# Kernel tuning notes

Hardware: AMD Instinct MI355X
Metric: run time of the kernel (lower is better)

## Reference

```python
import jax, jax.numpy as jnp
import numpy as np
import math

D_MODEL = 1024
N_HEAD = 16

def setup_inputs() -> dict:
    key = jax.random.key(0)
    ks = jax.random.split(key, 9)
    d = D_MODEL
    s = 0.02
    return {
        "x": jax.random.normal(ks[0], (4, 2048, d), dtype=jnp.float32),
        "Wq": jax.random.normal(ks[1], (d, d), dtype=jnp.float32) * s,
        "bq": jnp.zeros((d,), dtype=jnp.float32),
        "Wk": jax.random.normal(ks[2], (d, d), dtype=jnp.float32) * s,
        "bk": jnp.zeros((d,), dtype=jnp.float32),
        "Wv": jax.random.normal(ks[3], (d, d), dtype=jnp.float32) * s,
        "bv": jnp.zeros((d,), dtype=jnp.float32),
        "Wo": jax.random.normal(ks[4], (d, d), dtype=jnp.float32) * s,
        "bo": jnp.zeros((d,), dtype=jnp.float32),
    }

def reference(x, Wq, bq, Wk, bk, Wv, bv, Wo, bo):
    B, S, D = x.shape
    H = N_HEAD
    hd = D // H
    # linear projections (torch nn.Linear: x @ W.T + b), split heads -> [B,H,S,hd]
    def proj(W, b):
        return (jnp.einsum('bsd,ed->bse', x, W) + b).reshape(B, S, H, hd).transpose(0, 2, 1, 3)
    q = proj(Wq, bq)
    k = proj(Wk, bk)
    v = proj(Wv, bv)
    scale = 1.0 / math.sqrt(hd)
    att = jnp.einsum('bhqd,bhkd->bhqk', q, k) * scale  # [B,H,S,S]
    causal = jnp.tril(jnp.ones((S, S), dtype=bool))
    att = jnp.where(causal, att, jnp.float32(-jnp.inf))
    att = jax.nn.softmax(att, axis=-1)
    y = jnp.einsum('bhqk,bhkd->bhqd', att, v)  # [B,H,S,hd]
    y = y.transpose(0, 2, 1, 3).reshape(B, S, D)
    y = jnp.einsum('bsd,ed->bse', y, Wo) + bo  # dropout is identity in eval
    return y
```

## Files before the change

### kernel.cpp

```cpp
#include <hip/hip_runtime.h>

typedef unsigned short u16;
typedef __attribute__((ext_vector_type(4))) float f32x4;
typedef __attribute__((ext_vector_type(8))) __bf16 bf16x8;
typedef __attribute__((ext_vector_type(4))) unsigned int u32x4;

#define SEQ 2048
#define DMODEL 1024
#define HD 64
#define QKV_ELEMS 8388608

__device__ __forceinline__ u16 f2bf(float f) {
  unsigned int u = __builtin_bit_cast(unsigned int, f);
  u += 0x7FFFu + ((u >> 16) & 1u);
  return (u16)(u >> 16);
}

__device__ __forceinline__ void gl2lds16(const u16* g, u16* l) {
  __builtin_amdgcn_global_load_lds(
      (__attribute__((address_space(1))) void*)g,
      (__attribute__((address_space(3))) void*)l, 16, 0, 0);
}

__device__ __forceinline__ f32x4 mfma_bf(bf16x8 a, bf16x8 b, f32x4 c) {
  return __builtin_amdgcn_mfma_f32_16x16x32_bf16(a, b, c, 0, 0, 0);
}

__device__ __forceinline__ void lgkm0() {
  __asm__ volatile("s_waitcnt lgkmcnt(0)" ::: "memory");
}

__global__ __launch_bounds__(256) void prep(
    const float* __restrict__ x, const float* __restrict__ wq,
    const float* __restrict__ wk, const float* __restrict__ wv,
    const float* __restrict__ wo, u16* __restrict__ xb,
    u16* __restrict__ wqkvb, u16* __restrict__ wob) {
  int idx = blockIdx.x * 256 + threadIdx.x;
  const float* src;
  u16* dst;
  if (idx < 2097152) {
    src = x + (size_t)idx * 4;
    dst = xb + (size_t)idx * 4;
  } else {
    int j = idx - 2097152;
    int seg = j >> 18;
    int off = (j & 262143) * 4;
    if (seg == 0)      { src = wq + off; dst = wqkvb + off; }
    else if (seg == 1) { src = wk + off; dst = wqkvb + 1048576 + off; }
    else if (seg == 2) { src = wv + off; dst = wqkvb + 2097152 + off; }
    else               { src = wo + off; dst = wob + off; }
  }
  float4 f = *(const float4*)src;
  ushort4 o;
  o.x = f2bf(f.x); o.y = f2bf(f.y); o.z = f2bf(f.z); o.w = f2bf(f.w);
  *(ushort4*)dst = o;
}

template <int MODE>
__global__ __launch_bounds__(256) void gemm_bt(
    const u16* __restrict__ A, const u16* __restrict__ Bt,
    const float* __restrict__ b0, const float* __restrict__ b1,
    const float* __restrict__ b2, u16* __restrict__ outb,
    float* __restrict__ outf, int Ndim) {
  __shared__ u16 lS[8192];
  u16* lA = lS;
  u16* lB = lS + 4096;
  const int tid = threadIdx.x;
  const int w = tid >> 6, L = tid & 63;
  const int quad = L >> 4, lane16 = L & 15;
  const int wm = w >> 1, wn = w & 1;
  const int bm = blockIdx.x * 128, bn = blockIdx.y * 128;
  const int K = 1024;

  f32x4 acc[4][4];
  for (int i = 0; i < 4; ++i)
    for (int j = 0; j < 4; ++j)
      for (int r = 0; r < 4; ++r) acc[i][j][r] = 0.f;

  const int srow = L >> 2, scol = (L & 3) * 8;
  const u16* Ag = A + (size_t)(bm + w * 16 + srow) * K + scol;
  const u16* Bg = Bt + (size_t)(bn + w * 16 + srow) * K + scol;
  u16* lA0 = &lA[(w * 16) * 32];
  u16* lA1 = &lA[(64 + w * 16) * 32];
  u16* lB0 = &lB[(w * 16) * 32];
  u16* lB1 = &lB[(64 + w * 16) * 32];

  for (int k0 = 0; k0 < K; k0 += 32) {
    __syncthreads();
    gl2lds16(Ag + k0, lA0);
    gl2lds16(Ag + k0 + 64 * K, lA1);
    gl2lds16(Bg + k0, lB0);
    gl2lds16(Bg + k0 + 64 * K, lB1);
    __syncthreads();
    bf16x8 af[4], bfr[4];
    for (int mt = 0; mt < 4; ++mt)
      af[mt] = __builtin_bit_cast(
          bf16x8, *(const u32x4*)&lA[(wm * 64 + mt * 16 + lane16) * 32 + quad * 8]);
    for (int nt = 0; nt < 4; ++nt)
      bfr[nt] = __builtin_bit_cast(
          bf16x8, *(const u32x4*)&lB[(wn * 64 + nt * 16 + lane16) * 32 + quad * 8]);
    for (int mt = 0; mt < 4; ++mt)
      for (int nt = 0; nt < 4; ++nt)
        acc[mt][nt] = mfma_bf(af[mt], bfr[nt], acc[mt][nt]);
  }

  if (MODE == 0) {
    __syncthreads();
    const int n0 = bn + wn * 64;
    const int which = n0 >> 10;
    const int nn0 = n0 & 1023;
    const int h2 = nn0 >> 6;
    const int b = bm >> 11;
    const int bh = b * 16 + h2;
    const int sbase = (bm & 2047) + wm * 64;
    const float* bp = (which == 0) ? b0 : (which == 1) ? b1 : b2;
    const float scl = (which == 0) ? 0.125f : 1.0f;
    float bias[4];
    for (int nt = 0; nt < 4; ++nt) bias[nt] = bp[nn0 + nt * 16 + lane16];
    u16* buf = lS + w * 1152;

    for (int mt = 0; mt < 4; ++mt) {
      for (int nt = 0; nt < 4; ++nt)
        for (int r = 0; r < 4; ++r)
          buf[(quad * 4 + r) * 72 + nt * 16 + lane16] =
              f2bf((acc[mt][nt][r] + bias[nt]) * scl);
      lgkm0();
      const int sloc = sbase + mt * 16;
      if (which < 2) {
        const int sr = L >> 2, c = L & 3;
        u32x4 v0 = *(const u32x4*)&buf[sr * 72 + c * 16];
        u32x4 v1 = *(const u32x4*)&buf[sr * 72 + c * 16 + 8];
        u16* g = outb + (size_t)which * QKV_ELEMS +
                 ((size_t)bh * SEQ + sloc + sr) * HD + c * 16;
        *(u32x4*)g = v0;
        *(u32x4*)(g + 8) = v1;
      } else {
        u16 tmp[16] __attribute__((aligned(16)));
        for (int r = 0; r < 16; ++r) tmp[r] = buf[r * 72 + L];
        u16* g = outb + (size_t)2 * QKV_ELEMS +
                 ((size_t)bh * HD + L) * SEQ + sloc;
        *(u32x4*)g = *(const u32x4*)tmp;
        *(u32x4*)(g + 8) = *(const u32x4*)(tmp + 8);
      }
      lgkm0();
    }
  } else {
    for (int nt = 0; nt < 4; ++nt) {
      int n = bn + wn * 64 + nt * 16 + lane16;
      float bias = b0[n];
      for (int mt = 0; mt < 4; ++mt) {
        int m0 = bm + wm * 64 + mt * 16 + quad * 4;
        for (int r = 0; r < 4; ++r) {
          int m = m0 + r;
          outf[(size_t)m * Ndim + n] = acc[mt][nt][r] + bias;
        }
      }
    }
  }
}

__global__ __launch_bounds__(256, 2) void attn(
    const u16* __restrict__ Qb, const u16* __restrict__ Kb,
    const u16* __restrict__ VTb, u16* __restrict__ Yb) {
  __shared__ u16 lK[2][64 * 72];
  __shared__ u16 lVT[2][64 * 72];
  __shared__ u16 lP[4][32 * 72];
  const int tid = threadIdx.x;
  const int w = tid >> 6, L = tid & 63;
  const int quad = L >> 4, lane16 = L & 15;
  const int bh = blockIdx.y;
  const int b = bh >> 4, h = bh & 15;
  const int kr = tid >> 2, c = tid & 3;
  const u16* Kbase = Kb + (size_t)bh * SEQ * HD;
  const u16* VTbase = VTb + (size_t)bh * HD * SEQ;

  for (int phase = 0; phase < 2; ++phase) {
    const int qi = (phase == 0) ? (int)blockIdx.x : 15 - (int)blockIdx.x;
    const int qb = qi * 128;
    const int ntiles = 2 * qi + 2;
    const int wqmin = qb + w * 32;
    const int wqmax = wqmin + 31;

    u32x4 qf[2][2];
    for (int mt = 0; mt < 2; ++mt)
      for (int kh = 0; kh < 2; ++kh)
        qf[mt][kh] = *(const u32x4*)(Qb +
            ((size_t)bh * SEQ + qb + w * 32 + mt * 16 + lane16) * HD +
            kh * 32 + quad * 8);

    f32x4 o[2][4];
    float lsum[2][4];
    for (int mt = 0; mt < 2; ++mt)
      for (int r = 0; r < 4; ++r) lsum[mt][r] = 0.f;
    for (int mt = 0; mt < 2; ++mt)
      for (int dt = 0; dt < 4; ++dt)
        for (int r = 0; r < 4; ++r) o[mt][dt][r] = 0.f;

    u32x4 ka0, ka1, va0, va1;
    {
      const u16* ks = Kbase + (size_t)kr * HD + c * 16;
      ka0 = *(const u32x4*)ks;
      ka1 = *(const u32x4*)(ks + 8);
      const u16* vs = VTbase + (size_t)kr * SEQ + c * 16;
      va0 = *(const u32x4*)vs;
      va1 = *(const u32x4*)(vs + 8);
    }

    for (int it = 0; it < ntiles; ++it) {
      const int cur = it & 1;
      const int kj0 = it * 64;
      *(u32x4*)&lK[cur][kr * 72 + c * 16] = ka0;
      *(u32x4*)&lK[cur][kr * 72 + c * 16 + 8] = ka1;
      *(u32x4*)&lVT[cur][kr * 72 + c * 16] = va0;
      *(u32x4*)&lVT[cur][kr * 72 + c * 16 + 8] = va1;
      __syncthreads();
      if (it + 1 < ntiles) {
        const int kn = (it + 1) * 64;
        const u16* ks = Kbase + (size_t)(kn + kr) * HD + c * 16;
        ka0 = *(const u32x4*)ks;
        ka1 = *(const u32x4*)(ks + 8);
        const u16* vs = VTbase + (size_t)kr * SEQ + kn + c * 16;
        va0 = *(const u32x4*)vs;
        va1 = *(const u32x4*)(vs + 8);
      }
      if (kj0 > wqmax) continue;

      f32x4 s[2][4];
      for (int mt = 0; mt < 2; ++mt)
        for (int nt = 0; nt < 4; ++nt)
          for (int r = 0; r < 4; ++r) s[mt][nt][r] = 0.f;
      for (int nt = 0; nt < 4; ++nt) {
        bf16x8 k0 = __builtin_bit_cast(
            bf16x8, *(const u32x4*)&lK[cur][(nt * 16 + lane16) * 72 + quad * 8]);
        bf16x8 k1 = __builtin_bit_cast(
            bf16x8, *(const u32x4*)&lK[cur][(nt * 16 + lane16) * 72 + 32 + quad * 8]);
        for (int mt = 0; mt < 2; ++mt) {
          s[mt][nt] = mfma_bf(__builtin_bit_cast(bf16x8, qf[mt][0]), k0, s[mt][nt]);
          s[mt][nt] = mfma_bf(__builtin_bit_cast(bf16x8, qf[mt][1]), k1, s[mt][nt]);
        }
      }
      if (kj0 + 63 > wqmin) {
        for (int mt = 0; mt < 2; ++mt) {
          int qrow = wqmin + mt * 16 + quad * 4;
          for (int nt = 0; nt < 4; ++nt) {
            int kcol = kj0 + nt * 16 + lane16;
            for (int r = 0; r < 4; ++r)
              if (kcol > qrow + r) s[mt][nt][r] = -1e30f;
          }
        }
      }
      for (int mt = 0; mt < 2; ++mt)
        for (int nt = 0; nt < 4; ++nt)
          for (int r = 0; r < 4; ++r) {
            float p = __expf(s[mt][nt][r]);
            s[mt][nt][r] = p;
            lsum[mt][r] += p;
          }
      for (int mt = 0; mt < 2; ++mt)
        for (int nt = 0; nt < 4; ++nt)
          for (int r = 0; r < 4; ++r)
            lP[w][(mt * 16 + quad * 4 + r) * 72 + nt * 16 + lane16] =
                f2bf(s[mt][nt][r]);
      lgkm0();
      bf16x8 pf[2][2];
      for (int mt = 0; mt < 2; ++mt)
        for (int kt = 0; kt < 2; ++kt)
          pf[mt][kt] = __builtin_bit_cast(
              bf16x8,
              *(const u32x4*)&lP[w][(mt * 16 + lane16) * 72 + kt * 32 + quad * 8]);
      for (int dt = 0; dt < 4; ++dt) {
        bf16x8 v0 = __builtin_bit_cast(
            bf16x8, *(const u32x4*)&lVT[cur][(dt * 16 + lane16) * 72 + quad * 8]);
        bf16x8 v1 = __builtin_bit_cast(
            bf16x8, *(const u32x4*)&lVT[cur][(dt * 16 + lane16) * 72 + 32 + quad * 8]);
        for (int mt = 0; mt < 2; ++mt) {
          o[mt][dt] = mfma_bf(pf[mt][0], v0, o[mt][dt]);
          o[mt][dt] = mfma_bf(pf[mt][1], v1, o[mt][dt]);
        }
      }
    }
    __syncthreads();

    for (int mt = 0; mt < 2; ++mt)
      for (int xm = 1; xm <= 8; xm <<= 1)
        for (int r = 0; r < 4; ++r)
          lsum[mt][r] += __shfl_xor(lsum[mt][r], xm, 64);
    for (int mt = 0; mt < 2; ++mt) {
      float rl[4];
      for (int r = 0; r < 4; ++r) rl[r] = 1.0f / lsum[mt][r];
      for (int dt = 0; dt < 4; ++dt)
        for (int r = 0; r < 4; ++r) {
          int q = qb + w * 32 + mt * 16 + quad * 4 + r;
          Yb[((size_t)b * SEQ + q) * DMODEL + h * HD + dt * 16 + lane16] =
              f2bf(o[mt][dt][r] * rl[r]);
        }
    }
  }
}

extern "C" void kernel_launch(void* const* d_in, const int* in_sizes, int n_in,
                              void* d_out, int out_size, void* d_ws, size_t ws_size,
                              hipStream_t stream) {
  const float* x  = (const float*)d_in[0];
  const float* Wq = (const float*)d_in[1];
  const float* bq = (const float*)d_in[2];
  const float* Wk = (const float*)d_in[3];
  const float* bk = (const float*)d_in[4];
  const float* Wv = (const float*)d_in[5];
  const float* bv = (const float*)d_in[6];
  const float* Wo = (const float*)d_in[7];
  const float* bo = (const float*)d_in[8];
  float* out = (float*)d_out;

  char* ws = (char*)d_ws;
  u16* xb   = (u16*)ws;
  u16* wqkv = (u16*)(ws + 16777216);
  u16* wob  = (u16*)(ws + 23068672);
  u16* qbuf = (u16*)(ws + 25165824);
  u16* kbuf = qbuf + QKV_ELEMS;
  u16* vTbuf = qbuf + 2 * (size_t)QKV_ELEMS;
  u16* ybuf = xb;

  prep<<<12288, 256, 0, stream>>>(x, Wq, Wk, Wv, Wo, xb, wqkv, wob);
  gemm_bt<0><<<dim3(64, 24), 256, 0, stream>>>(xb, wqkv, bq, bk, bv, qbuf, nullptr, 3072);
  attn<<<dim3(8, 64), 256, 0, stream>>>(qbuf, kbuf, vTbuf, ybuf);
  gemm_bt<1><<<dim3(64, 8), 256, 0, stream>>>(ybuf, wob, bo, nullptr, nullptr, nullptr, out, 1024);
}
```

Before: 253.4 us.

## Transpose attention score tiles, use exp2 with folded scale, double-buffer GEMM epilogue

The attention kernel now computes S^T (keys as the MFMA A operand), so each lane holds four consecutive keys for one query. This lets P be packed into 64-bit LDS stores with truncating bf16 conversion, and lets the row sums reduce with fewer shuffles. The softmax uses a native exp2, with log2(e) folded into the Q projection scale. The QKV GEMM epilogue gets a separate double-buffered LDS staging area, drops a barrier, and transposes V with packed writes instead of scalar gathers. Truncating P to bf16 instead of rounding slightly changes numerics, and the extra 24KB of LDS may lower GEMM occupancy.

```diff
diff --git a/kernel.cpp b/kernel.cpp
--- a/kernel.cpp
+++ b/kernel.cpp
@@ -1,9 +1,11 @@
 #include <hip/hip_runtime.h>
 
 typedef unsigned short u16;
+typedef unsigned int u32;
 typedef __attribute__((ext_vector_type(4))) float f32x4;
 typedef __attribute__((ext_vector_type(8))) __bf16 bf16x8;
 typedef __attribute__((ext_vector_type(4))) unsigned int u32x4;
+typedef __attribute__((ext_vector_type(2))) unsigned int u32x2;
 
 #define SEQ 2048
 #define DMODEL 1024
@@ -11,9 +13,22 @@
 #define QKV_ELEMS 8388608
 
 __device__ __forceinline__ u16 f2bf(float f) {
-  unsigned int u = __builtin_bit_cast(unsigned int, f);
+  u32 u = __builtin_bit_cast(u32, f);
   u += 0x7FFFu + ((u >> 16) & 1u);
   return (u16)(u >> 16);
+}
+
+__device__ __forceinline__ u32 packtrunc(float a, float b) {
+  return (__builtin_bit_cast(u32, a) >> 16) |
+         (__builtin_bit_cast(u32, b) & 0xFFFF0000u);
+}
+
+__device__ __forceinline__ float fexp2(float x) {
+#if __has_builtin(__builtin_amdgcn_exp2f)
+  return __builtin_amdgcn_exp2f(x);
+#else
+  return __expf(x * 0.69314718056f);
+#endif
 }
 
 __device__ __forceinline__ void gl2lds16(const u16* g, u16* l) {
@@ -63,6 +78,7 @@
     const float* __restrict__ b2, u16* __restrict__ outb,
     float* __restrict__ outf, int Ndim) {
   __shared__ u16 lS[8192];
+  __shared__ u16 ebuf[12288];
   u16* lA = lS;
   u16* lB = lS + 4096;
   const int tid = threadIdx.x;
@@ -105,7 +121,6 @@
   }
 
   if (MODE == 0) {
-    __syncthreads();
     const int n0 = bn + wn * 64;
     const int which = n0 >> 10;
     const int nn0 = n0 & 1023;
@@ -114,19 +129,19 @@
     const int bh = b * 16 + h2;
     const int sbase = (bm & 2047) + wm * 64;
     const float* bp = (which == 0) ? b0 : (which == 1) ? b1 : b2;
-    const float scl = (which == 0) ? 0.125f : 1.0f;
+    const float scl = (which == 0) ? 0.18033688f : 1.0f;
     float bias[4];
     for (int nt = 0; nt < 4; ++nt) bias[nt] = bp[nn0 + nt * 16 + lane16];
-    u16* buf = lS + w * 1152;
 
     for (int mt = 0; mt < 4; ++mt) {
-      for (int nt = 0; nt < 4; ++nt)
-        for (int r = 0; r < 4; ++r)
-          buf[(quad * 4 + r) * 72 + nt * 16 + lane16] =
-              f2bf((acc[mt][nt][r] + bias[nt]) * scl);
-      lgkm0();
+      u16* buf = &ebuf[(mt & 1) * 6144 + w * 1536];
       const int sloc = sbase + mt * 16;
       if (which < 2) {
+        for (int nt = 0; nt < 4; ++nt)
+          for (int r = 0; r < 4; ++r)
+            buf[(quad * 4 + r) * 72 + nt * 16 + lane16] =
+                f2bf((acc[mt][nt][r] + bias[nt]) * scl);
+        lgkm0();
         const int sr = L >> 2, c = L & 3;
         u32x4 v0 = *(const u32x4*)&buf[sr * 72 + c * 16];
         u32x4 v1 = *(const u32x4*)&buf[sr * 72 + c * 16 + 8];
@@ -135,14 +150,21 @@
         *(u32x4*)g = v0;
         *(u32x4*)(g + 8) = v1;
       } else {
-        u16 tmp[16] __attribute__((aligned(16)));
-        for (int r = 0; r < 16; ++r) tmp[r] = buf[r * 72 + L];
+        for (int nt = 0; nt < 4; ++nt) {
+          u32 p0 = (u32)f2bf(acc[mt][nt][0] + bias[nt]) |
+                   ((u32)f2bf(acc[mt][nt][1] + bias[nt]) << 16);
+          u32 p1 = (u32)f2bf(acc[mt][nt][2] + bias[nt]) |
+                   ((u32)f2bf(acc[mt][nt][3] + bias[nt]) << 16);
+          *(u32x2*)&buf[(nt * 16 + lane16) * 24 + quad * 4] = (u32x2){p0, p1};
+        }
+        lgkm0();
+        u32x4 r0 = *(const u32x4*)&buf[L * 24];
+        u32x4 r1 = *(const u32x4*)&buf[L * 24 + 8];
         u16* g = outb + (size_t)2 * QKV_ELEMS +
                  ((size_t)bh * HD + L) * SEQ + sloc;
-        *(u32x4*)g = *(const u32x4*)tmp;
-        *(u32x4*)(g + 8) = *(const u32x4*)(tmp + 8);
-      }
-      lgkm0();
+        *(u32x4*)g = r0;
+        *(u32x4*)(g + 8) = r1;
+      }
     }
   } else {
     for (int nt = 0; nt < 4; ++nt) {
@@ -182,16 +204,15 @@
     const int wqmax = wqmin + 31;
 
     u32x4 qf[2][2];
-    for (int mt = 0; mt < 2; ++mt)
+    for (int qt = 0; qt < 2; ++qt)
       for (int kh = 0; kh < 2; ++kh)
-        qf[mt][kh] = *(const u32x4*)(Qb +
-            ((size_t)bh * SEQ + qb + w * 32 + mt * 16 + lane16) * HD +
+        qf[qt][kh] = *(const u32x4*)(Qb +
+            ((size_t)bh * SEQ + qb + w * 32 + qt * 16 + lane16) * HD +
             kh * 32 + quad * 8);
 
     f32x4 o[2][4];
-    float lsum[2][4];
-    for (int mt = 0; mt < 2; ++mt)
-      for (int r = 0; r < 4; ++r) lsum[mt][r] = 0.f;
+    float ls[2];
+    ls[0] = 0.f; ls[1] = 0.f;
     for (int mt = 0; mt < 2; ++mt)
       for (int dt = 0; dt < 4; ++dt)
         for (int r = 0; r < 4; ++r) o[mt][dt][r] = 0.f;
@@ -225,42 +246,42 @@
       }
       if (kj0 > wqmax) continue;
 
-      f32x4 s[2][4];
-      for (int mt = 0; mt < 2; ++mt)
-        for (int nt = 0; nt < 4; ++nt)
-          for (int r = 0; r < 4; ++r) s[mt][nt][r] = 0.f;
-      for (int nt = 0; nt < 4; ++nt) {
-        bf16x8 k0 = __builtin_bit_cast(
-            bf16x8, *(const u32x4*)&lK[cur][(nt * 16 + lane16) * 72 + quad * 8]);
-        bf16x8 k1 = __builtin_bit_cast(
-            bf16x8, *(const u32x4*)&lK[cur][(nt * 16 + lane16) * 72 + 32 + quad * 8]);
-        for (int mt = 0; mt < 2; ++mt) {
-          s[mt][nt] = mfma_bf(__builtin_bit_cast(bf16x8, qf[mt][0]), k0, s[mt][nt]);
-          s[mt][nt] = mfma_bf(__builtin_bit_cast(bf16x8, qf[mt][1]), k1, s[mt][nt]);
+      f32x4 sT[4][2];
+      for (int kt4 = 0; kt4 < 4; ++kt4)
+        for (int qt = 0; qt < 2; ++qt)
+          for (int r = 0; r < 4; ++r) sT[kt4][qt][r] = 0.f;
+      for (int kt4 = 0; kt4 < 4; ++kt4) {
+        bf16x8 kA0 = __builtin_bit_cast(
+            bf16x8, *(const u32x4*)&lK[cur][(kt4 * 16 + lane16) * 72 + quad * 8]);
+        bf16x8 kA1 = __builtin_bit_cast(
+            bf16x8, *(const u32x4*)&lK[cur][(kt4 * 16 + lane16) * 72 + 32 + quad * 8]);
+        for (int qt = 0; qt < 2; ++qt) {
+          sT[kt4][qt] = mfma_bf(kA0, __builtin_bit_cast(bf16x8, qf[qt][0]), sT[kt4][qt]);
+          sT[kt4][qt] = mfma_bf(kA1, __builtin_bit_cast(bf16x8, qf[qt][1]), sT[kt4][qt]);
         }
       }
       if (kj0 + 63 > wqmin) {
-        for (int mt = 0; mt < 2; ++mt) {
-          int qrow = wqmin + mt * 16 + quad * 4;
-          for (int nt = 0; nt < 4; ++nt) {
-            int kcol = kj0 + nt * 16 + lane16;
+        for (int kt4 = 0; kt4 < 4; ++kt4) {
+          int key0 = kj0 + kt4 * 16 + quad * 4;
+          for (int qt = 0; qt < 2; ++qt) {
+            int q = wqmin + qt * 16 + lane16;
             for (int r = 0; r < 4; ++r)
-              if (kcol > qrow + r) s[mt][nt][r] = -1e30f;
+              if (key0 + r > q) sT[kt4][qt][r] = -1e30f;
           }
         }
       }
-      for (int mt = 0; mt < 2; ++mt)
-        for (int nt = 0; nt < 4; ++nt)
-          for (int r = 0; r < 4; ++r) {
-            float p = __expf(s[mt][nt][r]);
-            s[mt][nt][r] = p;
-            lsum[mt][r] += p;
-          }
-      for (int mt = 0; mt < 2; ++mt)
-        for (int nt = 0; nt < 4; ++nt)
-          for (int r = 0; r < 4; ++r)
-            lP[w][(mt * 16 + quad * 4 + r) * 72 + nt * 16 + lane16] =
-                f2bf(s[mt][nt][r]);
+      for (int kt4 = 0; kt4 < 4; ++kt4)
+        for (int qt = 0; qt < 2; ++qt) {
+          float p0 = fexp2(sT[kt4][qt][0]);
+          float p1 = fexp2(sT[kt4][qt][1]);
+          float p2 = fexp2(sT[kt4][qt][2]);
+          float p3 = fexp2(sT[kt4][qt][3]);
+          ls[qt] += (p0 + p1) + (p2 + p3);
+          u32x2 pk;
+          pk.x = packtrunc(p0, p1);
+          pk.y = packtrunc(p2, p3);
+          *(u32x2*)&lP[w][(qt * 16 + lane16) * 72 + kt4 * 16 + quad * 4] = pk;
+        }
       lgkm0();
       bf16x8 pf[2][2];
       for (int mt = 0; mt < 2; ++mt)
@@ -281,13 +302,14 @@
     }
     __syncthreads();
 
-    for (int mt = 0; mt < 2; ++mt)
-      for (int xm = 1; xm <= 8; xm <<= 1)
-        for (int r = 0; r < 4; ++r)
-          lsum[mt][r] += __shfl_xor(lsum[mt][r], xm, 64);
+    for (int qt = 0; qt < 2; ++qt) {
+      ls[qt] += __shfl_xor(ls[qt], 16, 64);
+      ls[qt] += __shfl_xor(ls[qt], 32, 64);
+    }
     for (int mt = 0; mt < 2; ++mt) {
       float rl[4];
-      for (int r = 0; r < 4; ++r) rl[r] = 1.0f / lsum[mt][r];
+      for (int r = 0; r < 4; ++r)
+        rl[r] = 1.0f / __shfl(ls[mt], quad * 4 + r, 64);
       for (int dt = 0; dt < 4; ++dt)
         for (int r = 0; r < 4; ++r) {
           int q = qb + w * 32 + mt * 16 + quad * 4 + r;
```

Result: slower. 260.1 us (+2.6%).
